# Optimization experiments

Measured on AMD Instinct MI355X. Metric: run time of the kernel, lower is better.

## Reference

```python
import jax, jax.numpy as jnp
import numpy as np

NUM_TYPES = 8
TIME_DIM = 100
FEAT_DIM = 172
OUT_DIM = 128
E = 500000
D_IN = TIME_DIM + FEAT_DIM


def setup_inputs() -> dict:
    key = jax.random.key(0)
    k1, k2, k3, k4, k5, k6 = jax.random.split(key, 6)
    edge_feats = jax.random.normal(k1, (E, FEAT_DIM), dtype=jnp.float32)
    edge_ts = jax.random.uniform(k2, (E,), dtype=jnp.float32) * 1e4
    edge_types = jax.random.randint(k3, (E,), 0, NUM_TYPES, dtype=jnp.int64)
    # per-type Linear(time+feat -> out) weight stack, kaiming-ish init
    lim = 1.0 / np.sqrt(D_IN)
    W = jax.random.uniform(k4, (NUM_TYPES, D_IN, OUT_DIM), dtype=jnp.float32, minval=-lim, maxval=lim)
    b = jax.random.uniform(k5, (NUM_TYPES, OUT_DIM), dtype=jnp.float32, minval=-lim, maxval=lim)
    type_emb = jax.random.normal(k6, (NUM_TYPES, OUT_DIM), dtype=jnp.float32)
    return {"edge_feats": edge_feats, "edge_ts": edge_ts, "edge_types": edge_types,
            "W": W, "b": b, "type_emb": type_emb}


def reference(edge_feats, edge_ts, edge_types, W, b, type_emb):
    et = edge_types.astype(jnp.int32)
    # TimeEncode base frequencies (fixed, non-trainable): 1 / 10**linspace(0,9,dim)
    base_w = 1.0 / (10.0 ** jnp.linspace(0.0, 9.0, TIME_DIM, dtype=jnp.float32))  # [time_dim]
    mult = 1.0 + 0.1 * jnp.arange(NUM_TYPES, dtype=jnp.float32)                   # per-type freq multiplier
    w_per_edge = base_w[None, :] * mult[et][:, None]                              # [E, time_dim]
    time_feats = jnp.cos(edge_ts[:, None] * w_per_edge)                           # bias is zero
    combined = jnp.concatenate([edge_feats, time_feats], axis=1)                  # [E, D_in]
    out = jnp.zeros((combined.shape[0], OUT_DIM), dtype=jnp.float32)
    # per-edge-type masked dispatch: small fixed loop over NUM_TYPES
    for t in range(NUM_TYPES):
        mask = (et == t)[:, None]
        y = combined @ W[t] + b[t] + type_emb[t]
        out = jnp.where(mask, y, out)
    return out
```

## Files before the change

kernel.cpp:

```cpp
#include <hip/hip_runtime.h>
#include <hip/hip_bf16.h>

#define NT      8
#define TD      100
#define FEAT    172
#define DIN     272
#define KPAD    288
#define NKS     9
#define OUTD    128
#define BM      32
#define WIN     256
#define NST     (WIN / BM)
#define TWO_PI  6.283185307179586

typedef __bf16 bf16x8 __attribute__((ext_vector_type(8)));
typedef float  f32x4  __attribute__((ext_vector_type(4)));
typedef short  s16x8  __attribute__((ext_vector_type(8)));

__device__ __forceinline__ unsigned short f2bf(float f) {
    __hip_bfloat16 h = __float2bfloat16(f);
    return __builtin_bit_cast(unsigned short, h);
}

__global__ void k_detect(const int* __restrict__ words, int* __restrict__ flag) {
    __shared__ int s_or;
    if (threadIdx.x == 0) s_or = 0;
    __syncthreads();
    int v  = words[2 * threadIdx.x + 1];
    int v2 = words[2 * (threadIdx.x + 256) + 1];
    if (v | v2) atomicOr(&s_or, 1);
    __syncthreads();
    if (threadIdx.x == 0) *flag = (s_or == 0) ? 1 : 0;
}

__device__ __forceinline__ int get_type(const int* __restrict__ p, int e, int is64) {
    return p[is64 ? (2 * e) : e] & 7;
}

__global__ void k_prep_tables(const float* __restrict__ b, const float* __restrict__ temb,
                              float* __restrict__ freq_base, float* __restrict__ bias) {
    int gid = blockIdx.x * blockDim.x + threadIdx.x;
    if (gid < TD)
        freq_base[gid] = (float)(pow(10.0, -(double)gid / 11.0) / TWO_PI);
    if (gid < NT * OUTD) bias[gid] = b[gid] + temb[gid];
}

__global__ void k_prep_bfrag(const float* __restrict__ W, unsigned short* __restrict__ bfrag) {
    int gid = blockIdx.x * blockDim.x + threadIdx.x;
    if (gid >= NT * NKS * 8 * 64) return;
    int lane = gid & 63;
    int rest = gid >> 6;
    int nf = rest & 7; rest >>= 3;
    int s = rest % NKS, t = rest / NKS;
    int n  = nf * 16 + (lane & 15);
    int kb = s * 32 + (lane >> 4) * 8;
    unsigned short v[8];
    #pragma unroll
    for (int i = 0; i < 8; ++i) {
        int k = kb + i;
        float x = (k < DIN) ? W[((size_t)t * DIN + k) * OUTD + n] : 0.0f;
        v[i] = f2bf(x);
    }
    unsigned short* dst = bfrag + (size_t)gid * 8;
    #pragma unroll
    for (int i = 0; i < 8; ++i) dst[i] = v[i];
}

__global__ __launch_bounds__(512, 6) void k_main(
    const float* __restrict__ feats, const float* __restrict__ ts,
    const int* __restrict__ types, const int* __restrict__ flag,
    float* __restrict__ out, const float* __restrict__ freq_base,
    const float* __restrict__ bias_tab, const unsigned short* __restrict__ bfrag,
    int E)
{
    __shared__ __align__(16) unsigned short a_lds[2][2 * NKS * 64 * 8];
    __shared__ unsigned short pt[WIN];
    __shared__ float tsm[WIN];
    __shared__ float freq_lds[TD];
    __shared__ int cnt[NT];
    __shared__ int seg[NT + 1];
    __shared__ int um[NST];

    const int tid = threadIdx.x;
    const long base_e = (long)blockIdx.x * WIN;
    const int is64 = *flag;

    if (tid < NT)  cnt[tid] = 0;
    if (tid < NST) um[tid] = 0;
    if (tid < TD)  freq_lds[tid] = freq_base[tid];
    if (tid < WIN) { pt[tid] = 0xFFFF; tsm[tid] = 0.0f; }
    __syncthreads();

    int t0 = -1; float f0 = 0.f;
    if (tid < WIN) {
        long e0 = base_e + tid;
        if (e0 < (long)E) {
            t0 = get_type(types, (int)e0, is64);
            f0 = ts[e0] * (1.0f + 0.1f * (float)t0);
            atomicAdd(&cnt[t0], 1);
        }
    }
    __syncthreads();
    if (tid == 0) {
        int a = 0;
        #pragma unroll
        for (int t = 0; t < NT; ++t) { seg[t] = a; a += cnt[t]; cnt[t] = 0; }
        seg[NT] = a;
    }
    __syncthreads();
    if (t0 >= 0) {
        int r = seg[t0] + atomicAdd(&cnt[t0], 1);
        pt[r] = (unsigned short)(tid | (t0 << 12));
        tsm[r] = f0;
        atomicOr(&um[r >> 5], 1 << t0);
    }
    __syncthreads();

    const int g    = tid >> 8;
    const int tg   = tid & 255;
    const int w    = (tid >> 6) & 3;
    const int lane = tid & 63;
    const int hq = lane >> 4, l15 = lane & 15;
    const int col0 = w * 32 + l15;
    const int col1 = col0 + 16;

    #pragma unroll 1
    for (int i = 0; i <= NST; ++i) {
        if (i < NST && (i & 1) == g) {
            unsigned short* A = a_lds[g];
            const int rbase = i * BM;

            for (int idx = tg; idx < BM * 22; idx += 256) {
                int slot = idx / 22, kg = idx - slot * 22;
                unsigned p = pt[rbase + slot];
                float tm = tsm[rbase + slot];
                float4 fa = make_float4(0.f, 0.f, 0.f, 0.f);
                float4 fb = fa;
                if (p != 0xFFFFu) {
                    const float4* src = (const float4*)feats + (base_e + (p & 0xFF)) * 43;
                    fa = src[2 * kg];
                    if (kg < 21) fb = src[2 * kg + 1];
                }
                s16x8 v;
                v[0] = (short)f2bf(fa.x); v[1] = (short)f2bf(fa.y);
                v[2] = (short)f2bf(fa.z); v[3] = (short)f2bf(fa.w);
                if (kg < 21) {
                    v[4] = (short)f2bf(fb.x); v[5] = (short)f2bf(fb.y);
                    v[6] = (short)f2bf(fb.z); v[7] = (short)f2bf(fb.w);
                } else {
                    #pragma unroll
                    for (int q = 0; q < 4; ++q) {
                        float rev = tm * freq_lds[q];
                        float fr  = rev - floorf(rev);
                        v[4 + q] = (short)f2bf(__builtin_amdgcn_cosf(fr));
                    }
                }
                int s = kg >> 2, h = kg & 3;
                *(s16x8*)&A[(((slot >> 4) * NKS + s) * 64 + h * 16 + (slot & 15)) * 8] = v;
            }
            for (int idx = tg; idx < BM * 12; idx += 256) {
                int slot = idx & 31, gg = idx >> 5;
                float tm = tsm[rbase + slot];
                int kg = 22 + gg;
                int s = kg >> 2, h = kg & 3;
                int j0 = kg * 8 - FEAT;
                s16x8 v;
                #pragma unroll
                for (int q = 0; q < 8; ++q) {
                    float rev = tm * freq_lds[j0 + q];
                    float fr  = rev - floorf(rev);
                    v[q] = (short)f2bf(__builtin_amdgcn_cosf(fr));
                }
                *(s16x8*)&A[(((slot >> 4) * NKS + s) * 64 + h * 16 + (slot & 15)) * 8] = v;
            }
            for (int idx = tg; idx < BM * 2; idx += 256) {
                int slot = idx & 31, gg = idx >> 5;
                int kg = 34 + gg;
                int s = kg >> 2, h = kg & 3;
                s16x8 v = (s16x8){0, 0, 0, 0, 0, 0, 0, 0};
                *(s16x8*)&A[(((slot >> 4) * NKS + s) * 64 + h * 16 + (slot & 15)) * 8] = v;
            }
        }
        if (i >= 1 && ((i - 1) & 1) == g) {
            const unsigned short* A = a_lds[g];
            const int rbase = (i - 1) * BM;
            const int mask = um[i - 1];
            f32x4 acc[2][2];
            #pragma unroll 1
            for (int t = 0; t < NT; ++t) {
                if (!((mask >> t) & 1)) continue;
                #pragma unroll
                for (int rb = 0; rb < 2; ++rb) {
                    acc[rb][0] = (f32x4){0.f, 0.f, 0.f, 0.f};
                    acc[rb][1] = (f32x4){0.f, 0.f, 0.f, 0.f};
                }
                const s16x8* bp = (const s16x8*)bfrag + (size_t)t * NKS * 8 * 64;
                s16x8 nb0 = bp[(2 * w + 0) * 64 + lane];
                s16x8 nb1 = bp[(2 * w + 1) * 64 + lane];
                #pragma unroll 1
                for (int s = 0; s < NKS; ++s) {
                    s16x8 b0 = nb0, b1 = nb1;
                    if (s + 1 < NKS) {
                        nb0 = bp[((s + 1) * 8 + 2 * w + 0) * 64 + lane];
                        nb1 = bp[((s + 1) * 8 + 2 * w + 1) * 64 + lane];
                    }
                    bf16x8 bb0 = __builtin_bit_cast(bf16x8, b0);
                    bf16x8 bb1 = __builtin_bit_cast(bf16x8, b1);
                    #pragma unroll
                    for (int rb = 0; rb < 2; ++rb) {
                        s16x8 araw = *(const s16x8*)&A[((rb * NKS + s) * 64 + lane) * 8];
                        bf16x8 a = __builtin_bit_cast(bf16x8, araw);
                        acc[rb][0] = __builtin_amdgcn_mfma_f32_16x16x32_bf16(a, bb0, acc[rb][0], 0, 0, 0);
                        acc[rb][1] = __builtin_amdgcn_mfma_f32_16x16x32_bf16(a, bb1, acc[rb][1], 0, 0, 0);
                    }
                }
                const float bias0 = bias_tab[t * OUTD + col0];
                const float bias1 = bias_tab[t * OUTD + col1];
                #pragma unroll
                for (int rb = 0; rb < 2; ++rb)
                    #pragma unroll
                    for (int rg = 0; rg < 4; ++rg) {
                        unsigned p = pt[rbase + rb * 16 + hq * 4 + rg];
                        if ((int)(p >> 12) == t) {
                            long e = base_e + (p & 0xFF);
                            out[(size_t)e * OUTD + col0] = acc[rb][0][rg] + bias0;
                            out[(size_t)e * OUTD + col1] = acc[rb][1][rg] + bias1;
                        }
                    }
            }
        }
        __syncthreads();
    }
}

extern "C" void kernel_launch(void* const* d_in, const int* in_sizes, int n_in,
                              void* d_out, int out_size, void* d_ws, size_t ws_size,
                              hipStream_t stream) {
    const float* feats = (const float*)d_in[0];
    const float* ts    = (const float*)d_in[1];
    const int*   types = (const int*)d_in[2];
    const float* W     = (const float*)d_in[3];
    const float* b     = (const float*)d_in[4];
    const float* temb  = (const float*)d_in[5];
    float* out = (float*)d_out;
    const int E = in_sizes[1];

    char* ws = (char*)d_ws;
    auto align256 = [](size_t x) { return (x + 255) & ~(size_t)255; };
    int* flag = (int*)(ws + 0);
    size_t o = 256;
    float* freq_base = (float*)(ws + o); o = align256(o + TD * 4);
    float* bias      = (float*)(ws + o); o = align256(o + NT * OUTD * 4);
    unsigned short* bfrag = (unsigned short*)(ws + o);
    o = align256(o + (size_t)NT * NKS * 8 * 64 * 8 * 2);
    if (ws_size < o) return;

    k_detect<<<1, 256, 0, stream>>>(types, flag);
    k_prep_tables<<<8, 256, 0, stream>>>(b, temb, freq_base, bias);
    k_prep_bfrag<<<(NT * NKS * 8 * 64 + 255) / 256, 256, 0, stream>>>(W, bfrag);

    int nblocks = (E + WIN - 1) / WIN;
    k_main<<<nblocks, 512, 0, stream>>>(feats, ts, types, flag, out,
                                        freq_base, bias, bfrag, E);
}
```

Before: 230.2 us.

## Use all 8 waves for both staging and MFMA with register-prefetched feature loads

The block window grows from 256 to 512 edges, and the two-group split where half the block stages while the other half computes is removed. All eight waves now issue global feature loads into registers for the next 32-row tile, run the MFMA stage for the previous tile on 16 columns each, then convert and write the prefetched data to LDS. The intent is to hide global load latency behind the matrix work and keep every wave busy. In exchange the B fragments are held fully in registers per type, register pressure rises (launch bounds drop to 4 blocks), and each wave does half as many MFMAs per type.

```diff
diff --git a/kernel.cpp b/kernel.cpp
--- a/kernel.cpp
+++ b/kernel.cpp
@@ -9,7 +9,7 @@
 #define NKS     9
 #define OUTD    128
 #define BM      32
-#define WIN     256
+#define WIN     512
 #define NST     (WIN / BM)
 #define TWO_PI  6.283185307179586
 
@@ -66,7 +66,7 @@
     for (int i = 0; i < 8; ++i) dst[i] = v[i];
 }
 
-__global__ __launch_bounds__(512, 6) void k_main(
+__global__ __launch_bounds__(512, 4) void k_main(
     const float* __restrict__ feats, const float* __restrict__ ts,
     const int* __restrict__ types, const int* __restrict__ flag,
     float* __restrict__ out, const float* __restrict__ freq_base,
@@ -88,11 +88,12 @@
     if (tid < NT)  cnt[tid] = 0;
     if (tid < NST) um[tid] = 0;
     if (tid < TD)  freq_lds[tid] = freq_base[tid];
-    if (tid < WIN) { pt[tid] = 0xFFFF; tsm[tid] = 0.0f; }
+    pt[tid] = 0xFFFF;
+    tsm[tid] = 0.0f;
     __syncthreads();
 
     int t0 = -1; float f0 = 0.f;
-    if (tid < WIN) {
+    {
         long e0 = base_e + tid;
         if (e0 < (long)E) {
             t0 = get_type(types, (int)e0, is64);
@@ -116,38 +117,109 @@
     }
     __syncthreads();
 
-    const int g    = tid >> 8;
-    const int tg   = tid & 255;
-    const int w    = (tid >> 6) & 3;
-    const int lane = tid & 63;
+    if (tid < 128) {
+        int bufi = (tid >> 6) & 1, c = tid & 63;
+        int rb = (c >> 5) & 1, h = 2 + ((c >> 4) & 1), sl = c & 15;
+        s16x8 z = (s16x8){0, 0, 0, 0, 0, 0, 0, 0};
+        *(s16x8*)&a_lds[bufi][((rb * NKS + 8) * 64 + h * 16 + sl) * 8] = z;
+    }
+
+    const int w = tid >> 6, lane = tid & 63;
     const int hq = lane >> 4, l15 = lane & 15;
-    const int col0 = w * 32 + l15;
-    const int col1 = col0 + 16;
+    const int col = w * 16 + l15;
+
+    const int slotA = tid & 31, kgA = tid >> 5;
+    const int kgB   = 16 + (tid >> 5);
+    const bool hasB = (tid < 192);
+    const bool hasC = (tid < 384);
+
+    float4 fa0, fb0, fa1, fb1;
 
     #pragma unroll 1
     for (int i = 0; i <= NST; ++i) {
-        if (i < NST && (i & 1) == g) {
-            unsigned short* A = a_lds[g];
+        unsigned pA = 0xFFFFu, pB = 0xFFFFu;
+        if (i < NST) {
             const int rbase = i * BM;
-
-            for (int idx = tg; idx < BM * 22; idx += 256) {
-                int slot = idx / 22, kg = idx - slot * 22;
-                unsigned p = pt[rbase + slot];
-                float tm = tsm[rbase + slot];
-                float4 fa = make_float4(0.f, 0.f, 0.f, 0.f);
-                float4 fb = fa;
-                if (p != 0xFFFFu) {
-                    const float4* src = (const float4*)feats + (base_e + (p & 0xFF)) * 43;
-                    fa = src[2 * kg];
-                    if (kg < 21) fb = src[2 * kg + 1];
-                }
+            pA = pt[rbase + slotA];
+            fa0 = make_float4(0.f, 0.f, 0.f, 0.f); fb0 = fa0;
+            if (pA != 0xFFFFu) {
+                const float4* src = (const float4*)feats + (base_e + (pA & 0x1FF)) * 43;
+                fa0 = src[2 * kgA]; fb0 = src[2 * kgA + 1];
+            }
+            if (hasB) {
+                pB = pt[rbase + slotA];
+                fa1 = make_float4(0.f, 0.f, 0.f, 0.f); fb1 = fa1;
+                if (pB != 0xFFFFu) {
+                    const float4* src = (const float4*)feats + (base_e + (pB & 0x1FF)) * 43;
+                    fa1 = src[2 * kgB];
+                    if (kgB < 21) fb1 = src[2 * kgB + 1];
+                }
+            }
+        }
+
+        if (i >= 1) {
+            const unsigned short* A = a_lds[(i - 1) & 1];
+            const int rbase = (i - 1) * BM;
+            const int mask = um[i - 1];
+            if (mask) {
+                unsigned pm0[4], pm1[4];
+                #pragma unroll
+                for (int rg = 0; rg < 4; ++rg) {
+                    pm0[rg] = pt[rbase + hq * 4 + rg];
+                    pm1[rg] = pt[rbase + 16 + hq * 4 + rg];
+                }
+                #pragma unroll 1
+                for (int t = 0; t < NT; ++t) {
+                    if (!((mask >> t) & 1)) continue;
+                    const s16x8* bp = (const s16x8*)bfrag + ((size_t)t * NKS * 8 + w) * 64 + lane;
+                    s16x8 breg[NKS];
+                    #pragma unroll
+                    for (int s = 0; s < NKS; ++s) breg[s] = bp[s * 8 * 64];
+                    f32x4 acc0 = (f32x4){0.f, 0.f, 0.f, 0.f};
+                    f32x4 acc1 = (f32x4){0.f, 0.f, 0.f, 0.f};
+                    #pragma unroll
+                    for (int s = 0; s < NKS; ++s) {
+                        bf16x8 bb = __builtin_bit_cast(bf16x8, breg[s]);
+                        s16x8 a0 = *(const s16x8*)&A[((0 * NKS + s) * 64 + lane) * 8];
+                        s16x8 a1 = *(const s16x8*)&A[((1 * NKS + s) * 64 + lane) * 8];
+                        acc0 = __builtin_amdgcn_mfma_f32_16x16x32_bf16(
+                            __builtin_bit_cast(bf16x8, a0), bb, acc0, 0, 0, 0);
+                        acc1 = __builtin_amdgcn_mfma_f32_16x16x32_bf16(
+                            __builtin_bit_cast(bf16x8, a1), bb, acc1, 0, 0, 0);
+                    }
+                    const float bias = bias_tab[t * OUTD + col];
+                    #pragma unroll
+                    for (int rg = 0; rg < 4; ++rg) {
+                        if ((int)(pm0[rg] >> 12) == t)
+                            out[(size_t)(base_e + (pm0[rg] & 0x1FF)) * OUTD + col] = acc0[rg] + bias;
+                        if ((int)(pm1[rg] >> 12) == t)
+                            out[(size_t)(base_e + (pm1[rg] & 0x1FF)) * OUTD + col] = acc1[rg] + bias;
+                    }
+                }
+            }
+        }
+
+        if (i < NST) {
+            unsigned short* A = (unsigned short*)a_lds[i & 1];
+            const int rbase = i * BM;
+            {
                 s16x8 v;
-                v[0] = (short)f2bf(fa.x); v[1] = (short)f2bf(fa.y);
-                v[2] = (short)f2bf(fa.z); v[3] = (short)f2bf(fa.w);
-                if (kg < 21) {
-                    v[4] = (short)f2bf(fb.x); v[5] = (short)f2bf(fb.y);
-                    v[6] = (short)f2bf(fb.z); v[7] = (short)f2bf(fb.w);
+                v[0] = (short)f2bf(fa0.x); v[1] = (short)f2bf(fa0.y);
+                v[2] = (short)f2bf(fa0.z); v[3] = (short)f2bf(fa0.w);
+                v[4] = (short)f2bf(fb0.x); v[5] = (short)f2bf(fb0.y);
+                v[6] = (short)f2bf(fb0.z); v[7] = (short)f2bf(fb0.w);
+                int s = kgA >> 2, h = kgA & 3;
+                *(s16x8*)&A[(((slotA >> 4) * NKS + s) * 64 + h * 16 + (slotA & 15)) * 8] = v;
+            }
+            if (hasB) {
+                s16x8 v;
+                v[0] = (short)f2bf(fa1.x); v[1] = (short)f2bf(fa1.y);
+                v[2] = (short)f2bf(fa1.z); v[3] = (short)f2bf(fa1.w);
+                if (kgB < 21) {
+                    v[4] = (short)f2bf(fb1.x); v[5] = (short)f2bf(fb1.y);
+                    v[6] = (short)f2bf(fb1.z); v[7] = (short)f2bf(fb1.w);
                 } else {
+                    float tm = tsm[rbase + slotA];
                     #pragma unroll
                     for (int q = 0; q < 4; ++q) {
                         float rev = tm * freq_lds[q];
@@ -155,14 +227,12 @@
                         v[4 + q] = (short)f2bf(__builtin_amdgcn_cosf(fr));
                     }
                 }
-                int s = kg >> 2, h = kg & 3;
-                *(s16x8*)&A[(((slot >> 4) * NKS + s) * 64 + h * 16 + (slot & 15)) * 8] = v;
-            }
-            for (int idx = tg; idx < BM * 12; idx += 256) {
-                int slot = idx & 31, gg = idx >> 5;
+                int s = kgB >> 2, h = kgB & 3;
+                *(s16x8*)&A[(((slotA >> 4) * NKS + s) * 64 + h * 16 + (slotA & 15)) * 8] = v;
+            }
+            if (hasC) {
+                int slot = tid & 31, kg = 22 + (tid >> 5);
                 float tm = tsm[rbase + slot];
-                int kg = 22 + gg;
-                int s = kg >> 2, h = kg & 3;
                 int j0 = kg * 8 - FEAT;
                 s16x8 v;
                 #pragma unroll
@@ -171,62 +241,8 @@
                     float fr  = rev - floorf(rev);
                     v[q] = (short)f2bf(__builtin_amdgcn_cosf(fr));
                 }
+                int s = kg >> 2, h = kg & 3;
                 *(s16x8*)&A[(((slot >> 4) * NKS + s) * 64 + h * 16 + (slot & 15)) * 8] = v;
-            }
-            for (int idx = tg; idx < BM * 2; idx += 256) {
-                int slot = idx & 31, gg = idx >> 5;
-                int kg = 34 + gg;
-                int s = kg >> 2, h = kg & 3;
-                s16x8 v = (s16x8){0, 0, 0, 0, 0, 0, 0, 0};
-                *(s16x8*)&A[(((slot >> 4) * NKS + s) * 64 + h * 16 + (slot & 15)) * 8] = v;
-            }
-        }
-        if (i >= 1 && ((i - 1) & 1) == g) {
-            const unsigned short* A = a_lds[g];
-            const int rbase = (i - 1) * BM;
-            const int mask = um[i - 1];
-            f32x4 acc[2][2];
-            #pragma unroll 1
-            for (int t = 0; t < NT; ++t) {
-                if (!((mask >> t) & 1)) continue;
-                #pragma unroll
-                for (int rb = 0; rb < 2; ++rb) {
-                    acc[rb][0] = (f32x4){0.f, 0.f, 0.f, 0.f};
-                    acc[rb][1] = (f32x4){0.f, 0.f, 0.f, 0.f};
-                }
-                const s16x8* bp = (const s16x8*)bfrag + (size_t)t * NKS * 8 * 64;
-                s16x8 nb0 = bp[(2 * w + 0) * 64 + lane];
-                s16x8 nb1 = bp[(2 * w + 1) * 64 + lane];
-                #pragma unroll 1
-                for (int s = 0; s < NKS; ++s) {
-                    s16x8 b0 = nb0, b1 = nb1;
-                    if (s + 1 < NKS) {
-                        nb0 = bp[((s + 1) * 8 + 2 * w + 0) * 64 + lane];
-                        nb1 = bp[((s + 1) * 8 + 2 * w + 1) * 64 + lane];
-                    }
-                    bf16x8 bb0 = __builtin_bit_cast(bf16x8, b0);
-                    bf16x8 bb1 = __builtin_bit_cast(bf16x8, b1);
-                    #pragma unroll
-                    for (int rb = 0; rb < 2; ++rb) {
-                        s16x8 araw = *(const s16x8*)&A[((rb * NKS + s) * 64 + lane) * 8];
-                        bf16x8 a = __builtin_bit_cast(bf16x8, araw);
-                        acc[rb][0] = __builtin_amdgcn_mfma_f32_16x16x32_bf16(a, bb0, acc[rb][0], 0, 0, 0);
-                        acc[rb][1] = __builtin_amdgcn_mfma_f32_16x16x32_bf16(a, bb1, acc[rb][1], 0, 0, 0);
-                    }
-                }
-                const float bias0 = bias_tab[t * OUTD + col0];
-                const float bias1 = bias_tab[t * OUTD + col1];
-                #pragma unroll
-                for (int rb = 0; rb < 2; ++rb)
-                    #pragma unroll
-                    for (int rg = 0; rg < 4; ++rg) {
-                        unsigned p = pt[rbase + rb * 16 + hq * 4 + rg];
-                        if ((int)(p >> 12) == t) {
-                            long e = base_e + (p & 0xFF);
-                            out[(size_t)e * OUTD + col0] = acc[rb][0][rg] + bias0;
-                            out[(size_t)e * OUTD + col1] = acc[rb][1][rg] + bias1;
-                        }
-                    }
             }
         }
         __syncthreads();
```

After: 210.9 us. -8.4%, faster.
